# Optimization experiments

Hardware: AMD Instinct MI355X
Metric: run time of the kernel (lower is better)

## Reference

```python
import jax, jax.numpy as jnp
import numpy as np

NUM_EMBEDDINGS = 1024
EMBEDDING_DIM = 256
COMMITMENT_COST = 0.25


def setup_inputs() -> dict:
    key = jax.random.key(0)
    k_z, k_e = jax.random.split(key)
    z = jax.random.normal(k_z, (8, EMBEDDING_DIM, 16, 16, 16), dtype=jnp.float32)
    # nn.Embedding weight initialized uniform(-1/K, 1/K)
    codebook = jax.random.uniform(
        k_e, (NUM_EMBEDDINGS, EMBEDDING_DIM), dtype=jnp.float32,
        minval=-1.0 / NUM_EMBEDDINGS, maxval=1.0 / NUM_EMBEDDINGS)
    return {"z": z, "codebook": codebook}


def reference(z, codebook):
    B, D, H, W, L = z.shape
    # (B, D, H, W, L) -> (B, H, W, L, D) -> (N, D)
    z_perm = jnp.transpose(z, (0, 2, 3, 4, 1))          # (B,H,W,L,D)
    z_flat = z_perm.reshape(-1, D)                       # (N,D)
    # squared-distance via expansion: ||z||^2 + ||e||^2 - 2 z.e^T
    distances = ((z_flat ** 2).sum(axis=1, keepdims=True)
                 + (codebook ** 2).sum(axis=1)
                 - 2.0 * z_flat @ codebook.T)            # (N,K)
    indices = jnp.argmin(distances, axis=1)              # (N,)
    quantized = codebook[indices].reshape(B, H, W, L, D)
    idx_out = indices.reshape(B, H, W, L)
    # losses (stop_gradient mirrors .detach())
    e_latent_loss = jnp.mean((jax.lax.stop_gradient(quantized) - z_perm) ** 2)
    q_latent_loss = jnp.mean((quantized - jax.lax.stop_gradient(z_perm)) ** 2)
    vq_loss = q_latent_loss + COMMITMENT_COST * e_latent_loss
    # straight-through estimator
    quant_st = z_perm + jax.lax.stop_gradient(quantized - z_perm)
    quant_out = jnp.transpose(quant_st, (0, 4, 1, 2, 3))  # (B,D,H,W,L)
    return quant_out, idx_out, vq_loss
```

## Files before the change

### kernel.cpp

```cpp
#include <hip/hip_runtime.h>


#define K_CODES 1024
#define DIM 256
#define N_TOK 32768
#define SPATIAL 4096
#define TOK_BLK 64
#define NBLK (N_TOK / TOK_BLK)
#define CAP 28
#define MARGIN 1e-3f

typedef __attribute__((ext_vector_type(8))) short short8;
typedef __attribute__((ext_vector_type(4))) float float4v;

#define WS_LOSS 0
#define WS_CNT 8
#define WS_E2 16
#define WS_EB 2048

#define O_IDX (8 * DIM * SPATIAL)
#define O_LOSS (O_IDX + N_TOK)

__device__ __forceinline__ short f2bf(float v) {
  unsigned u = __float_as_uint(v);
  u = (u + 0x7fffu + ((u >> 16) & 1u)) >> 16;
  return (short)u;
}

__device__ __forceinline__ void gload_lds16(const void* g, void* l) {
  __builtin_amdgcn_global_load_lds(
      (__attribute__((address_space(1))) unsigned*)g,
      (__attribute__((address_space(3))) unsigned*)l, 16, 0, 0);
}

__device__ __forceinline__ void stage_issue(const uint4* eBg, short* lbuf,
                                            int stage, int tid) {
#pragma unroll
  for (int i = 0; i < 8; i++)
    gload_lds16(eBg + (size_t)stage * 2048 + i * 256 + tid,
                lbuf + ((i * 256 + tid) << 3));
}

__global__ __launch_bounds__(256) void prep_kernel(const float* __restrict__ e,
                                                   float* __restrict__ ws) {
  __shared__ float sq[DIM];
  __shared__ __align__(16) short sbf[DIM];
  __shared__ float chv[16];
  int k = blockIdx.x, d = threadIdx.x;
  float v = e[k * DIM + d];
  sbf[d] = f2bf(v);
  sq[d] = __fmul_rn(v, v);
  __syncthreads();
  if (d < 32) {
    int f = d >> 2, q = d & 3;
    int stage = k >> 6, ct = (k >> 4) & 3, nn = k & 15;
    short8 chunk = *(const short8*)(sbf + f * 32 + q * 8);
    int off8 = ((stage * 4 + ct) * 8 + f) * 64 + q * 16 + nn;
    ((short8*)(ws + WS_EB))[off8] = chunk;
  }
  if (d < 16) {
    int blkb = d >> 3, j = d & 7;
    const float* x = sq + blkb * 128;
    float c = x[j];
#pragma unroll
    for (int i = 1; i < 16; i++) c = __fadd_rn(c, x[i * 8 + j]);
    chv[d] = c;
  }
  __syncthreads();
  if (d == 0) {
    float a0 = __fadd_rn(__fadd_rn(chv[0], chv[1]), __fadd_rn(chv[2], chv[3]));
    float a1 = __fadd_rn(__fadd_rn(chv[4], chv[5]), __fadd_rn(chv[6], chv[7]));
    float resA = __fadd_rn(a0, a1);
    float b0 = __fadd_rn(__fadd_rn(chv[8], chv[9]), __fadd_rn(chv[10], chv[11]));
    float b1 = __fadd_rn(__fadd_rn(chv[12], chv[13]), __fadd_rn(chv[14], chv[15]));
    float resB = __fadd_rn(b0, b1);
    ws[WS_E2 + k] = __fadd_rn(resA, resB);
    if (k == 0) {
      ws[WS_LOSS] = 0.f;
      ((unsigned*)ws)[WS_CNT] = 0u;
    }
  }
}

__global__ __launch_bounds__(256, 2) void main_kernel(const float* __restrict__ z,
                                                      const float* __restrict__ e,
                                                      float* __restrict__ ws,
                                                      float* __restrict__ out) {
  __shared__ __align__(16) short Bst[2][64 * 256];
  __shared__ unsigned short cand[TOK_BLK][CAP];
  __shared__ float cands[TOK_BLK][CAP];
  __shared__ float aminv[TOK_BLK];
  __shared__ int cnt[TOK_BLK];
  __shared__ float Szs[TOK_BLK];
  __shared__ int mini_sh[TOK_BLK];
  __shared__ float red[4];

  int tid = threadIdx.x, w = tid >> 6, lane = tid & 63;
  int quad = lane >> 4, nn = lane & 15;
  int n0 = blockIdx.x * TOK_BLK;
  int b = n0 >> 12, s0 = n0 & 4095;
  const float* zb = z + (size_t)b * DIM * SPATIAL + s0;
  const float* Se = ws + WS_E2;
  const uint4* eBg = (const uint4*)(ws + WS_EB);
  if (tid < TOK_BLK) cnt[tid] = 0;

  stage_issue(eBg, Bst[0], 0, tid);
  stage_issue(eBg, Bst[1], 1, tid);
  __builtin_amdgcn_sched_barrier(0);

  {
    const float* zp = zb + w * 16 + nn;
    float r[4];
#pragma unroll
    for (int t = 0; t < 4; t++) {
      int c = quad * 4 + t, blkb = c >> 3, j = c & 7;
      float v0 = zp[(size_t)(blkb * 128 + j) * SPATIAL];
      r[t] = __fmul_rn(v0, v0);
      for (int i = 1; i < 16; i++) {
        float vv = zp[(size_t)(blkb * 128 + i * 8 + j) * SPATIAL];
        r[t] = __fadd_rn(r[t], __fmul_rn(vv, vv));
      }
    }
    float half = __fadd_rn(__fadd_rn(r[0], r[1]), __fadd_rn(r[2], r[3]));
    float other = __shfl_xor(half, 16);
    float resb = __fadd_rn(half, other);
    float res_o = __shfl_xor(resb, 32);
    float total = __fadd_rn(resb, res_o);
    if (quad == 0) Szs[w * 16 + nn] = total;
  }

  int tokA = w * 16 + nn;
  short8 A[8];
#pragma unroll
  for (int f = 0; f < 8; f++) {
    short8 a;
#pragma unroll
    for (int j = 0; j < 8; j++) {
      int d = f * 32 + quad * 8 + j;
      a[j] = f2bf(zb[(size_t)d * SPATIAL + tokA]);
    }
    A[f] = a;
  }

  __syncthreads();

  float thr[4] = {3.4e38f, 3.4e38f, 3.4e38f, 3.4e38f};
  for (int stage = 0; stage < 16; stage++) {
    if (stage == 15) {
      asm volatile("s_waitcnt vmcnt(0)" ::: "memory");
    } else {
      asm volatile("s_waitcnt vmcnt(8)" ::: "memory");
    }
    __builtin_amdgcn_sched_barrier(0);
    __builtin_amdgcn_s_barrier();
    const short* Bbuf = Bst[stage & 1];

    for (int ct = 0; ct < 4; ct++) {
      int kbase = stage * 64 + ct * 16;
      float4v C = {0.f, 0.f, 0.f, 0.f};
      const short8* Bp = (const short8*)Bbuf + ct * 8 * 64;
#pragma unroll
      for (int f = 0; f < 8; f++) {
        short8 Bf = Bp[f * 64 + lane];
        C = __builtin_amdgcn_mfma_f32_16x16x32_bf16(A[f], Bf, C, 0, 0, 0);
      }
      float SeK = Se[kbase + nn];
      float sv[4];
      bool pr[4];
#pragma unroll
      for (int r = 0; r < 4; r++) {
        float s = fmaf(-2.f, C[r], SeK);
        float m = s;
        m = fminf(m, __shfl_xor(m, 1, 16));
        m = fminf(m, __shfl_xor(m, 2, 16));
        m = fminf(m, __shfl_xor(m, 4, 16));
        m = fminf(m, __shfl_xor(m, 8, 16));
        thr[r] = fminf(thr[r], m);
        sv[r] = s;
        pr[r] = s < thr[r] + MARGIN;
      }
      if (__ballot(pr[0] | pr[1] | pr[2] | pr[3])) {
#pragma unroll
        for (int r = 0; r < 4; r++) {
          unsigned long long bl = __ballot(pr[r]);
          unsigned grp = (unsigned)((bl >> (quad * 16)) & 0xffffULL);
          if (grp) {
            int tb = w * 16 + quad * 4 + r;
            int base = cnt[tb];
            if (pr[r]) {
              int pos = base + __popc(grp & ((1u << nn) - 1u));
              if (pos < CAP) {
                cand[tb][pos] = (unsigned short)(kbase + nn);
                cands[tb][pos] = sv[r];
              }
            }
            if (nn == 0) cnt[tb] = base + __popc(grp);
          }
        }
      }
    }

    __builtin_amdgcn_s_barrier();
    if (stage < 14) stage_issue(eBg, Bst[stage & 1], stage + 2, tid);
    __builtin_amdgcn_sched_barrier(0);
  }
#pragma unroll
  for (int r = 0; r < 4; r++)
    if (nn == 0) aminv[w * 16 + quad * 4 + r] = thr[r];

  int tb = w * 16 + nn;
  int cc = cnt[tb];
  int cl = cc < CAP ? cc : CAP;
  float bestD = 3.4e38f;
  int bestk = 0x7fffffff;
  {
    const float* zp = zb + tb;
    float amin = aminv[tb], Szn = Szs[tb];
    for (int c = quad; c < cl; c += 4) {
      if (cands[tb][c] >= amin + MARGIN) continue;
      int k = cand[tb][c];
      const float* er = e + (size_t)k * DIM;
      float acc = 0.f;
#pragma unroll 8
      for (int d = 0; d < DIM; d++) acc = fmaf(zp[(size_t)d * SPATIAL], er[d], acc);
      float D = __fsub_rn(__fadd_rn(Szn, Se[k]), __fmul_rn(2.f, acc));
      if (D < bestD || (D == bestD && k < bestk)) { bestD = D; bestk = k; }
    }
  }
#pragma unroll
  for (int off = 32; off >= 16; off >>= 1) {
    float oD = __shfl_down(bestD, off);
    int ok = __shfl_down(bestk, off);
    if (oD < bestD || (oD == bestD && ok < bestk)) { bestD = oD; bestk = ok; }
  }
  if (lane < 16 && cnt[w * 16 + lane] <= CAP) {
    mini_sh[w * 16 + lane] = bestk;
    out[O_IDX + n0 + w * 16 + lane] = (float)bestk;
  }
  for (int t = 0; t < 16; t++) {
    int tb2 = w * 16 + t;
    if (cnt[tb2] > CAP) {
      const float* zq = zb + tb2;
      float Szn = Szs[tb2];
      float bD = 3.4e38f;
      int bk = 0x7fffffff;
      for (int k = lane; k < K_CODES; k += 64) {
        const float* er = e + (size_t)k * DIM;
        float acc = 0.f;
#pragma unroll 8
        for (int d = 0; d < DIM; d++) acc = fmaf(zq[(size_t)d * SPATIAL], er[d], acc);
        float D = __fsub_rn(__fadd_rn(Szn, Se[k]), __fmul_rn(2.f, acc));
        if (D < bD || (D == bD && k < bk)) { bD = D; bk = k; }
      }
#pragma unroll
      for (int m = 1; m < 64; m <<= 1) {
        float oD = __shfl_xor(bD, m);
        int ok = __shfl_xor(bk, m);
        if (oD < bD || (oD == bD && ok < bk)) { bD = oD; bk = ok; }
      }
      if (lane == 0) {
        mini_sh[tb2] = bk;
        out[O_IDX + n0 + tb2] = (float)bk;
      }
    }
  }
  __syncthreads();

  int mten = mini_sh[lane];
  const float* erow = e + (size_t)mten * DIM;
  float* op = out + (size_t)b * DIM * SPATIAL + s0;
  float sumsq = 0.f;
  for (int i = 0; i < 64; i++) {
    int d = w * 64 + i;
    float v = erow[d];
    float zv = zb[(size_t)d * SPATIAL + lane];
    float df = __fsub_rn(v, zv);
    sumsq = fmaf(df, df, sumsq);
    op[(size_t)d * SPATIAL + lane] = v;
  }
#pragma unroll
  for (int o = 32; o > 0; o >>= 1) sumsq += __shfl_down(sumsq, o, 64);
  if (lane == 0) red[w] = sumsq;
  __syncthreads();
  if (tid == 0) {
    atomicAdd(ws + WS_LOSS, red[0] + red[1] + red[2] + red[3]);
    __threadfence();
    unsigned t = atomicAdd((unsigned*)ws + WS_CNT, 1u);
    if (t == NBLK - 1) {
      float total = atomicAdd(ws + WS_LOSS, 0.f);
      out[O_LOSS] = 1.25f * total / 8388608.f;
    }
  }
}

extern "C" void kernel_launch(void* const* d_in, const int* in_sizes, int n_in,
                              void* d_out, int out_size, void* d_ws, size_t ws_size,
                              hipStream_t stream) {
  const float* z = (const float*)d_in[0];
  const float* e = (const float*)d_in[1];
  float* ws = (float*)d_ws;
  float* out = (float*)d_out;

  prep_kernel<<<K_CODES, 256, 0, stream>>>(e, ws);
  main_kernel<<<NBLK, 256, 0, stream>>>(z, e, ws, out);
}
```

Before: 219.2 us.

## Single-buffer codebook staging and vectorize codebook row loads with float4

Replaces the double-buffered asynchronous LDS staging of bf16 codebook tiles with a single buffer that is loaded synchronously each stage between two barriers. This halves the shared-memory footprint, which may allow more resident blocks. The cost is that global-load latency is no longer overlapped with MFMA work. Codebook row reads in the candidate rescoring, the fallback full search and the output/loss loop now use float4 loads, cutting the number of load instructions.

Measured after the change: 210.8 us. 1.04x faster.

```diff
diff --git a/kernel.cpp b/kernel.cpp
--- a/kernel.cpp
+++ b/kernel.cpp
@@ -86,7 +86,7 @@
                                                       const float* __restrict__ e,
                                                       float* __restrict__ ws,
                                                       float* __restrict__ out) {
-  __shared__ __align__(16) short Bst[2][64 * 256];
+  __shared__ __align__(16) short Bst[64 * 256];
   __shared__ unsigned short cand[TOK_BLK][CAP];
   __shared__ float cands[TOK_BLK][CAP];
   __shared__ float aminv[TOK_BLK];
@@ -104,10 +104,6 @@
   const uint4* eBg = (const uint4*)(ws + WS_EB);
   if (tid < TOK_BLK) cnt[tid] = 0;
 
-  stage_issue(eBg, Bst[0], 0, tid);
-  stage_issue(eBg, Bst[1], 1, tid);
-  __builtin_amdgcn_sched_barrier(0);
-
   {
     const float* zp = zb + w * 16 + nn;
     float r[4];
@@ -142,23 +138,16 @@
     A[f] = a;
   }
 
-  __syncthreads();
-
   float thr[4] = {3.4e38f, 3.4e38f, 3.4e38f, 3.4e38f};
   for (int stage = 0; stage < 16; stage++) {
-    if (stage == 15) {
-      asm volatile("s_waitcnt vmcnt(0)" ::: "memory");
-    } else {
-      asm volatile("s_waitcnt vmcnt(8)" ::: "memory");
-    }
-    __builtin_amdgcn_sched_barrier(0);
-    __builtin_amdgcn_s_barrier();
-    const short* Bbuf = Bst[stage & 1];
+    __syncthreads();
+    stage_issue(eBg, Bst, stage, tid);
+    __syncthreads();
 
     for (int ct = 0; ct < 4; ct++) {
       int kbase = stage * 64 + ct * 16;
       float4v C = {0.f, 0.f, 0.f, 0.f};
-      const short8* Bp = (const short8*)Bbuf + ct * 8 * 64;
+      const short8* Bp = (const short8*)Bst + ct * 8 * 64;
 #pragma unroll
       for (int f = 0; f < 8; f++) {
         short8 Bf = Bp[f * 64 + lane];
@@ -199,10 +188,6 @@
         }
       }
     }
-
-    __builtin_amdgcn_s_barrier();
-    if (stage < 14) stage_issue(eBg, Bst[stage & 1], stage + 2, tid);
-    __builtin_amdgcn_sched_barrier(0);
   }
 #pragma unroll
   for (int r = 0; r < 4; r++)
@@ -221,8 +206,14 @@
       int k = cand[tb][c];
       const float* er = e + (size_t)k * DIM;
       float acc = 0.f;
-#pragma unroll 8
-      for (int d = 0; d < DIM; d++) acc = fmaf(zp[(size_t)d * SPATIAL], er[d], acc);
+#pragma unroll 4
+      for (int dd = 0; dd < DIM; dd += 4) {
+        float4 e4 = *(const float4*)(er + dd);
+        acc = fmaf(zp[(size_t)(dd + 0) * SPATIAL], e4.x, acc);
+        acc = fmaf(zp[(size_t)(dd + 1) * SPATIAL], e4.y, acc);
+        acc = fmaf(zp[(size_t)(dd + 2) * SPATIAL], e4.z, acc);
+        acc = fmaf(zp[(size_t)(dd + 3) * SPATIAL], e4.w, acc);
+      }
       float D = __fsub_rn(__fadd_rn(Szn, Se[k]), __fmul_rn(2.f, acc));
       if (D < bestD || (D == bestD && k < bestk)) { bestD = D; bestk = k; }
     }
@@ -247,8 +238,14 @@
       for (int k = lane; k < K_CODES; k += 64) {
         const float* er = e + (size_t)k * DIM;
         float acc = 0.f;
-#pragma unroll 8
-        for (int d = 0; d < DIM; d++) acc = fmaf(zq[(size_t)d * SPATIAL], er[d], acc);
+#pragma unroll 4
+        for (int dd = 0; dd < DIM; dd += 4) {
+          float4 e4 = *(const float4*)(er + dd);
+          acc = fmaf(zq[(size_t)(dd + 0) * SPATIAL], e4.x, acc);
+          acc = fmaf(zq[(size_t)(dd + 1) * SPATIAL], e4.y, acc);
+          acc = fmaf(zq[(size_t)(dd + 2) * SPATIAL], e4.z, acc);
+          acc = fmaf(zq[(size_t)(dd + 3) * SPATIAL], e4.w, acc);
+        }
         float D = __fsub_rn(__fadd_rn(Szn, Se[k]), __fmul_rn(2.f, acc));
         if (D < bD || (D == bD && k < bk)) { bD = D; bk = k; }
       }
@@ -270,13 +267,18 @@
   const float* erow = e + (size_t)mten * DIM;
   float* op = out + (size_t)b * DIM * SPATIAL + s0;
   float sumsq = 0.f;
-  for (int i = 0; i < 64; i++) {
-    int d = w * 64 + i;
-    float v = erow[d];
-    float zv = zb[(size_t)d * SPATIAL + lane];
-    float df = __fsub_rn(v, zv);
-    sumsq = fmaf(df, df, sumsq);
-    op[(size_t)d * SPATIAL + lane] = v;
+#pragma unroll 4
+  for (int i4 = 0; i4 < 64; i4 += 4) {
+    int d = w * 64 + i4;
+    float4 v4 = *(const float4*)(erow + d);
+#pragma unroll
+    for (int m = 0; m < 4; m++) {
+      float v = (m == 0) ? v4.x : (m == 1) ? v4.y : (m == 2) ? v4.z : v4.w;
+      float zv = zb[(size_t)(d + m) * SPATIAL + lane];
+      float df = __fsub_rn(v, zv);
+      sumsq = fmaf(df, df, sumsq);
+      op[(size_t)(d + m) * SPATIAL + lane] = v;
+    }
   }
 #pragma unroll
   for (int o = 32; o > 0; o >>= 1) sumsq += __shfl_down(sumsq, o, 64);
```
